# Performance work log

Measured on AMD Instinct MI355X. Metric: run time of the kernel, lower is better.

## Reference

```python
import jax, jax.numpy as jnp
import numpy as np

# physics constants (match init_kwargs)
DT = 1.0 / 60.0
G_ACC = 9.81
RHO = 1.225
CD = 0.47
NU = 0.001
B, N, GRID = 512, 64, 16


def _norm(x):
    return jnp.linalg.norm(x, axis=-1, keepdims=True)


def _deriv(pos, vel, rot, omega, mass, inertia, contacts, fluid_v,
           Fext, tau, log_A, log_k, log_b, conv_w):
    g_vec = jnp.array([0.0, 0.0, -G_ACC], dtype=pos.dtype)
    Fg = mass[..., None] * g_vec                                  # [B,N,3]
    A = jax.nn.softplus(log_A).reshape(1, -1, 1)
    vm = jnp.maximum(_norm(vel), 1e-6)
    Fd = -0.5 * RHO * CD * A * vm * vel                           # drag
    k = jax.nn.softplus(log_k)
    b = jax.nn.softplus(log_b)
    d_ij = pos[:, None, :, :] - pos[:, :, None, :]                # [B,N,N,3] = p_j - p_i
    dist = jnp.maximum(_norm(d_ij), 1e-6)
    n_hat = d_ij / dist
    pen = jax.nn.relu(1.0 - dist[..., 0])                         # penetration depth
    dvel = vel[:, None, :, :] - vel[:, :, None, :]                # v_j - v_i
    Fc = (k * pen[..., None] * n_hat + b * dvel * contacts[..., None]).sum(axis=2)
    dv = (Fext + Fg + Fd + Fc) / mass[..., None]
    Io = inertia * omega
    domega = (tau - jnp.cross(omega, Io)) / jnp.maximum(inertia, 1e-6)
    w, x, y, z = rot[..., 0], rot[..., 1], rot[..., 2], rot[..., 3]
    ox, oy, oz = omega[..., 0], omega[..., 1], omega[..., 2]
    drot = 0.5 * jnp.stack([
        -x * ox - y * oy - z * oz,
        w * ox + y * oz - z * oy,
        w * oy - x * oz + z * ox,
        w * oz + x * oy - y * ox], axis=-1)
    P_in = (Fext * vel).sum((-1, -2))
    P_dis = -(Fd * vel).sum((-1, -2))
    dE = P_in - P_dis
    Bsz = fluid_v.shape[0]
    u = fluid_v.reshape(Bsz, GRID, GRID, GRID, 3).transpose(0, 4, 1, 2, 3)  # NCDHW
    dfluid = NU * jax.lax.conv_general_dilated(
        u, conv_w, window_strides=(1, 1, 1), padding=[(1, 1)] * 3,
        feature_group_count=3,
        dimension_numbers=('NCDHW', 'OIDHW', 'NCDHW'))
    dfluid = dfluid.transpose(0, 2, 3, 4, 1).reshape(Bsz, GRID ** 3, 3)
    return vel, dv, drot, domega, dE, dfluid


def _quat_normalize(q):
    return q / jnp.maximum(_norm(q), 1e-12)


def _apply(pos, vel, rot, omega, fluid_v, dt, dp, dv, dr, dw, dfluid):
    npos = pos + dt * dp
    nvel = vel + dt * dv
    nrot = _quat_normalize(rot + dt * dr)
    nomega = omega + dt * dw
    new_u = fluid_v + dt * dfluid
    nfluid = new_u - new_u.mean(axis=1, keepdims=True)
    return npos, nvel, nrot, nomega, nfluid


def _forward(pos, vel, rot, omega, mass, inertia, contacts, energy, fluid_v,
             Fext, tau, log_A, log_k, log_b, conv_w):
    dt = DT
    params = (mass, inertia, contacts)

    def deriv(p, v, r, o, fv):
        return _deriv(p, v, r, o, mass, inertia, contacts, fv,
                      Fext, tau, log_A, log_k, log_b, conv_w)

    k1 = deriv(pos, vel, rot, omega, fluid_v)
    s2 = _apply(pos, vel, rot, omega, fluid_v, dt / 2, k1[0], k1[1], k1[2], k1[3], k1[5])
    k2 = deriv(*s2)
    s3 = _apply(pos, vel, rot, omega, fluid_v, dt / 2, k2[0], k2[1], k2[2], k2[3], k2[5])
    k3 = deriv(*s3)
    s4 = _apply(pos, vel, rot, omega, fluid_v, dt, k3[0], k3[1], k3[2], k3[3], k3[5])
    k4 = deriv(*s4)

    def rk4c(y, a, b_, c, d):
        return y + dt / 6 * (a + 2 * b_ + 2 * c + d)

    npos = rk4c(pos, k1[0], k2[0], k3[0], k4[0])
    nvel = rk4c(vel, k1[1], k2[1], k3[1], k4[1])
    nrot = _quat_normalize(rk4c(rot, k1[2], k2[2], k3[2], k4[2]))
    nomega = rk4c(omega, k1[3], k2[3], k3[3], k4[3])
    nenergy = rk4c(energy, k1[4], k2[4], k3[4], k4[4])
    nforces = Fext + mass[..., None] * k1[1]
    raw_fluid = rk4c(fluid_v, k1[5], k2[5], k3[5], k4[5])
    nfluid = raw_fluid - raw_fluid.mean(axis=1, keepdims=True)
    Bsz = pos.shape[0]
    # flatten new state: [pos, vel, rot, omega, forces, energy, fluid_v]
    return jnp.concatenate([
        npos.reshape(Bsz, -1), nvel.reshape(Bsz, -1), nrot.reshape(Bsz, -1),
        nomega.reshape(Bsz, -1), nforces.reshape(Bsz, -1),
        nenergy[:, None], nfluid.reshape(Bsz, -1)], axis=-1)


def setup_inputs() -> dict:
    key = jax.random.key(0)
    ks = jax.random.split(key, 12)
    rot = jax.random.normal(ks[2], (B, N, 4), dtype=jnp.float32)
    rot = rot / jnp.maximum(jnp.linalg.norm(rot, axis=-1, keepdims=True), 1e-12)
    return {
        'pos': 2.0 * jax.random.normal(ks[0], (B, N, 3), dtype=jnp.float32),
        'vel': jax.random.normal(ks[1], (B, N, 3), dtype=jnp.float32),
        'rot': rot,
        'omega': jax.random.normal(ks[3], (B, N, 3), dtype=jnp.float32),
        'mass': 0.5 + jax.random.uniform(ks[4], (B, N), dtype=jnp.float32),
        'inertia': 0.05 + 0.1 * jax.random.uniform(ks[5], (B, N, 3), dtype=jnp.float32),
        'contacts': jax.random.uniform(ks[6], (B, N, N), dtype=jnp.float32),
        'energy': jnp.zeros((B,), dtype=jnp.float32),
        'fluid_v': jax.random.normal(ks[7], (B, GRID ** 3, 3), dtype=jnp.float32),
        'Fext': jax.random.normal(ks[8], (B, N, 3), dtype=jnp.float32),
        'tau': jax.random.normal(ks[9], (B, N, 3), dtype=jnp.float32),
        'log_A': jnp.zeros((N,), dtype=jnp.float32),
        'log_k': jnp.full((1,), np.log(1000.0), dtype=jnp.float32),
        'log_b': jnp.full((1,), np.log(10.0), dtype=jnp.float32),
        'conv_w': 0.1 * jax.random.normal(ks[10], (3, 1, 3, 3, 3), dtype=jnp.float32),
    }


def reference(pos, vel, rot, omega, mass, inertia, contacts, energy, fluid_v,
              Fext, tau, log_A, log_k, log_b, conv_w):
    return _forward(pos, vel, rot, omega, mass, inertia, contacts, energy,
                    fluid_v, Fext, tau, log_A, log_k, log_b, conv_w)
```

## Files before the change

kernel.cpp:

```cpp
#include <hip/hip_runtime.h>

#define DT (1.0f/60.0f)
#define G_ACC 9.81f
#define RHO 1.225f
#define CD_ 0.47f
#define NU 0.001f

__device__ __forceinline__ float softplus_f(float x) {
    return log1pf(expf(-fabsf(x))) + fmaxf(x, 0.0f);
}

#define RL(v, l) __int_as_float(__builtin_amdgcn_readlane(__float_as_int(v), (l)))
#define SLANE(x) __int_as_float(__builtin_amdgcn_readfirstlane(__float_as_int(x)))

__device__ __forceinline__ float dpp_xm(float v) {
    return __int_as_float(__builtin_amdgcn_update_dpp(0, __float_as_int(v), 0x111, 0xf, 0xf, true));
}
__device__ __forceinline__ float dpp_xp(float v) {
    return __int_as_float(__builtin_amdgcn_update_dpp(0, __float_as_int(v), 0x101, 0xf, 0xf, true));
}

__global__ __launch_bounds__(512) void fused_kernel(
    const float* __restrict__ pos, const float* __restrict__ vel,
    const float* __restrict__ rot, const float* __restrict__ omega,
    const float* __restrict__ mass, const float* __restrict__ inertia,
    const float* __restrict__ contacts, const float* __restrict__ energy,
    const float* __restrict__ fluid, const float* __restrict__ Fext,
    const float* __restrict__ tau, const float* __restrict__ log_A,
    const float* __restrict__ log_k, const float* __restrict__ log_b,
    const float* __restrict__ conv_w, float* __restrict__ out)
{
    __shared__ float smem[8772];
    const int t = threadIdx.x;

    if (blockIdx.x < 1536) {
        const int b   = blockIdx.x & 511;
        const int ch  = blockIdx.x >> 9;
        const int col = t & 255;
        const int h   = t >> 8;
        const int x   = col & 15, y = col >> 4, wv = t >> 6;
        const int h8  = h << 3;
        float* red = smem + 8740;

        float W[27];
        #pragma unroll
        for (int k = 0; k < 27; ++k) W[k] = NU * SLANE(conv_w[ch*27 + k]);

        const int lb = col*17;
        if (t < 18) { smem[4352 + t] = 0.f; smem[4370 + 4352 + t] = 0.f; }

        const float* fb = fluid + (size_t)b*12288 + 3*col + ch;
        float base[8], acc[8];
        #pragma unroll
        for (int zz = 0; zz < 8; ++zz) {
            float v = fb[(h8 + zz)*768];
            base[zz] = v; acc[zz] = 0.f;
            smem[lb + h8 + zz] = v;
        }

        const float xm = (x > 0) ? 1.f : 0.f, xp = (x < 15) ? 1.f : 0.f;
        const float mm = (y > 0) ? 1.f : 0.f, pm = (y < 15) ? 1.f : 0.f;
        float Sdz0, Sdz1, Sdz2;
        {
            float a0 = W[0]*xm + W[1] + W[2]*xp;
            float a1 = W[3]*xm + W[4] + W[5]*xp;
            float a2 = W[6]*xm + W[7] + W[8]*xp;
            Sdz0 = mm*a0 + a1 + pm*a2;
            a0 = W[ 9]*xm + W[10] + W[11]*xp;
            a1 = W[12]*xm + W[13] + W[14]*xp;
            a2 = W[15]*xm + W[16] + W[17]*xp;
            Sdz1 = mm*a0 + a1 + pm*a2;
            a0 = W[18]*xm + W[19] + W[20]*xp;
            a1 = W[21]*xm + W[22] + W[23]*xp;
            a2 = W[24]*xm + W[25] + W[26]*xp;
            Sdz2 = mm*a0 + a1 + pm*a2;
        }
        const float SzLo = Sdz1 + Sdz2;
        const float SzHi = Sdz0 + Sdz1;
        const float SzMid = Sdz0 + Sdz1 + Sdz2;

        const int ownR = lb + h8 - 1;
        const int cmR  = (y > 0)  ? (lb - 272 + h8 - 1) : 4353;
        const int cpR  = (y < 15) ? (lb + 272 + h8 - 1) : 4353;

        __syncthreads();
        float mean = 0.f;

        #define LOADC(cidx) { \
            const float* Up = smem + rb + (cidx); \
            if (h == 0) { c[0] = 0.f; \
                _Pragma("unroll") for (int k = 1; k < 10; ++k) c[k] = Up[k]; } \
            else { \
                _Pragma("unroll") for (int k = 0; k < 9; ++k) c[k] = Up[k]; \
                c[9] = 0.f; } }

        #define SCAT(wy) { \
            _Pragma("unroll") for (int k = 0; k < 10; ++k) { \
                float cc = c[k], cl = dpp_xm(cc), cr = dpp_xp(cc); \
                if (k < 8) \
                    o[k]   += W[(wy)*3+0]*cl + W[(wy)*3+1]*cc + W[(wy)*3+2]*cr; \
                if (k >= 1 && k <= 8) \
                    o[k-1] += W[9+(wy)*3+0]*cl + W[9+(wy)*3+1]*cc + W[9+(wy)*3+2]*cr; \
                if (k >= 2) \
                    o[k-2] += W[18+(wy)*3+0]*cl + W[18+(wy)*3+1]*cc + W[18+(wy)*3+2]*cr; \
            } }

        #pragma unroll
        for (int s = 0; s < 4; ++s) {
            const int rb = (s & 1) * 4370;
            const int wb = 4370 - rb;
            float o[8];
            #pragma unroll
            for (int zz = 0; zz < 8; ++zz) o[zz] = 0.f;
            {
                float c[10];
                LOADC(ownR); SCAT(1);
                LOADC(cmR);  SCAT(0);
                LOADC(cpR);  SCAT(2);
            }

            if (s < 3) {
                const float hstep = (s == 2) ? DT : DT*0.5f;
                const float w = (s == 0) ? 1.f : 2.f;
                float ps = 0.f;
                #pragma unroll
                for (int zz = 0; zz < 8; ++zz) {
                    float Sz = (h == 0 && zz == 0) ? SzLo
                             : ((h == 1 && zz == 7) ? SzHi : SzMid);
                    float k = o[zz] - mean * Sz;
                    acc[zz] += w * k;
                    float v = base[zz] + hstep * k;
                    smem[wb + lb + h8 + zz] = v;
                    ps += v;
                }
                #pragma unroll
                for (int off = 32; off > 0; off >>= 1) ps += __shfl_xor(ps, off, 64);
                if ((t & 63) == 0) red[s*8 + wv] = ps;
                __syncthreads();
                mean = (red[s*8+0]+red[s*8+1]+red[s*8+2]+red[s*8+3]
                       +red[s*8+4]+red[s*8+5]+red[s*8+6]+red[s*8+7]) * (1.0f/4096.0f);
            } else {
                #pragma unroll
                for (int zz = 0; zz < 8; ++zz) {
                    float Sz = (h == 0 && zz == 0) ? SzLo
                             : ((h == 1 && zz == 7) ? SzHi : SzMid);
                    acc[zz] += o[zz] - mean * Sz;
                }
            }
        }
        #undef LOADC
        #undef SCAT

        float raw[8], ps = 0.f;
        #pragma unroll
        for (int zz = 0; zz < 8; ++zz) { raw[zz] = base[zz] + (DT/6.0f)*acc[zz]; ps += raw[zz]; }
        #pragma unroll
        for (int off = 32; off > 0; off >>= 1) ps += __shfl_xor(ps, off, 64);
        if ((t & 63) == 0) red[24 + wv] = ps;
        __syncthreads();
        const float mn = (red[24]+red[25]+red[26]+red[27]
                         +red[28]+red[29]+red[30]+red[31]) * (1.0f/4096.0f);

        float* ob = out + (size_t)b*13313 + 1025 + 3*col + ch;
        #pragma unroll
        for (int zz = 0; zz < 8; ++zz) ob[(h8 + zz)*768] = raw[zz] - mn;
        return;
    }

    const int b = blockIdx.x - 1536;
    const int q = t >> 6;
    const int i = t & 63;
    float* cont = smem;
    float* sF   = smem + 4160;

    {
        const float4* cg = (const float4*)(contacts + (size_t)b*4096);
        #pragma unroll
        for (int v = 0; v < 2; ++v) {
            float4 c4 = cg[v*512 + t];
            int fi = (v*512 + t) * 4;
            int r = fi >> 6, cc = fi & 63;
            float* p = cont + r*65 + cc;
            p[0] = c4.x; p[1] = c4.y; p[2] = c4.z; p[3] = c4.w;
        }
    }

    const size_t p3 = ((size_t)b*64 + i)*3;
    const size_t p4 = ((size_t)b*64 + i)*4;
    float bpx=pos[p3],   bpy=pos[p3+1],   bpz=pos[p3+2];
    float bvx=vel[p3],   bvy=vel[p3+1],   bvz=vel[p3+2];
    float brw=rot[p4],   brx=rot[p4+1],   bry=rot[p4+2],  brz=rot[p4+3];
    float box=omega[p3], boy=omega[p3+1], boz=omega[p3+2];
    float m  = mass[(size_t)b*64+i];
    float Ix=inertia[p3], Iy=inertia[p3+1], Iz=inertia[p3+2];
    float Fex=Fext[p3],   Fey=Fext[p3+1],   Fez=Fext[p3+2];
    float tx=tau[p3],     ty=tau[p3+1],     tz=tau[p3+2];
    float dragc = -0.5f * RHO * CD_ * softplus_f(log_A[i]);
    float kc = softplus_f(SLANE(log_k[0]));
    float bc = softplus_f(SLANE(log_b[0]));
    float invm = 1.0f / m;
    float iIx = 1.0f/fmaxf(Ix,1e-6f), iIy = 1.0f/fmaxf(Iy,1e-6f), iIz = 1.0f/fmaxf(Iz,1e-6f);

    float cpx=bpx, cpy=bpy, cpz=bpz;
    float cvx=bvx, cvy=bvy, cvz=bvz;
    float crw=brw, crx=brx, cry=bry, crz=brz;
    float cox=box, coy=boy, coz=boz;

    float apx=0,apy=0,apz=0, avx=0,avy=0,avz=0;
    float arw=0,arx=0,ary=0,arz=0, awx=0,awy=0,awz=0;
    float eacc=0.f;

    const int j0 = q << 3;
    float* ob = out + (size_t)b * 13313;
    __syncthreads();

    #pragma unroll
    for (int s = 0; s < 4; ++s) {
        float Fcx=0.f, Fcy=0.f, Fcz=0.f;
        #pragma unroll
        for (int jj = 0; jj < 8; ++jj) {
            const int j = j0 + jj;
            float pjx = RL(cpx, j), pjy = RL(cpy, j), pjz = RL(cpz, j);
            float vjx = RL(cvx, j), vjy = RL(cvy, j), vjz = RL(cvz, j);
            float dx = pjx - cpx, dy = pjy - cpy, dz = pjz - cpz;
            float dist = fmaxf(sqrtf(dx*dx + dy*dy + dz*dz), 1e-6f);
            float pen  = fmaxf(1.0f - dist, 0.0f);
            float coef = kc * pen * __builtin_amdgcn_rcpf(dist);
            float cbj  = bc * cont[i*65 + j];
            Fcx += coef*dx + cbj*(vjx - cvx);
            Fcy += coef*dy + cbj*(vjy - cvy);
            Fcz += coef*dz + cbj*(vjz - cvz);
        }
        sF[q*192 + i*3+0] = Fcx;
        sF[q*192 + i*3+1] = Fcy;
        sF[q*192 + i*3+2] = Fcz;
        __syncthreads();
        Fcx = 0.f; Fcy = 0.f; Fcz = 0.f;
        #pragma unroll
        for (int qq = 0; qq < 8; ++qq) {
            Fcx += sF[qq*192 + i*3+0];
            Fcy += sF[qq*192 + i*3+1];
            Fcz += sF[qq*192 + i*3+2];
        }

        float vm = fmaxf(sqrtf(cvx*cvx+cvy*cvy+cvz*cvz), 1e-6f);
        float dc = dragc * vm;
        float Fdx = dc*cvx, Fdy = dc*cvy, Fdz = dc*cvz;

        float dvx = (Fex + Fdx + Fcx) * invm;
        float dvy = (Fey + Fdy + Fcy) * invm;
        float dvz = (Fez - m*G_ACC + Fdz + Fcz) * invm;

        if (s == 0 && q == 0) {
            ob[832 + i*3+0] = Fex + m*dvx;
            ob[832 + i*3+1] = Fey + m*dvy;
            ob[832 + i*3+2] = Fez + m*dvz;
        }

        float dqw = 0.5f*(-crx*cox - cry*coy - crz*coz);
        float dqx = 0.5f*( crw*cox + cry*coz - crz*coy);
        float dqy = 0.5f*( crw*coy - crx*coz + crz*cox);
        float dqz = 0.5f*( crw*coz + crx*coy - cry*cox);

        float Iox = Ix*cox, Ioy = Iy*coy, Ioz = Iz*coz;
        float dwx = (tx - (coy*Ioz - coz*Ioy)) * iIx;
        float dwy = (ty - (coz*Iox - cox*Ioz)) * iIy;
        float dwz = (tz - (cox*Ioy - coy*Iox)) * iIz;

        float ei = (Fex+Fdx)*cvx + (Fey+Fdy)*cvy + (Fez+Fdz)*cvz;
        #pragma unroll
        for (int off = 32; off > 0; off >>= 1) ei += __shfl_xor(ei, off, 64);

        const float w = (s == 0 || s == 3) ? 1.f : 2.f;
        eacc += w * ei;
        apx += w*cvx; apy += w*cvy; apz += w*cvz;
        avx += w*dvx; avy += w*dvy; avz += w*dvz;
        arw += w*dqw; arx += w*dqx; ary += w*dqy; arz += w*dqz;
        awx += w*dwx; awy += w*dwy; awz += w*dwz;

        if (s < 3) {
            const float h = (s == 2) ? DT : DT*0.5f;
            float npx = bpx + h*cvx, npy = bpy + h*cvy, npz = bpz + h*cvz;
            cvx = bvx + h*dvx; cvy = bvy + h*dvy; cvz = bvz + h*dvz;
            cpx = npx; cpy = npy; cpz = npz;
            float qw = brw + h*dqw, qx = brx + h*dqx, qy = bry + h*dqy, qz = brz + h*dqz;
            float iqn = 1.0f / fmaxf(sqrtf(qw*qw+qx*qx+qy*qy+qz*qz), 1e-12f);
            crw = qw*iqn; crx = qx*iqn; cry = qy*iqn; crz = qz*iqn;
            cox = box + h*dwx; coy = boy + h*dwy; coz = boz + h*dwz;
            __syncthreads();
        }
    }

    if (q == 0) {
        const float s6 = DT / 6.0f;
        ob[      i*3+0] = bpx + s6*apx;  ob[      i*3+1] = bpy + s6*apy;  ob[      i*3+2] = bpz + s6*apz;
        ob[192 + i*3+0] = bvx + s6*avx;  ob[192 + i*3+1] = bvy + s6*avy;  ob[192 + i*3+2] = bvz + s6*avz;
        {
            float qw=brw+s6*arw, qx=brx+s6*arx, qy=bry+s6*ary, qz=brz+s6*arz;
            float iq = 1.0f / fmaxf(sqrtf(qw*qw+qx*qx+qy*qy+qz*qz), 1e-12f);
            ob[384 + i*4+0]=qw*iq; ob[384 + i*4+1]=qx*iq; ob[384 + i*4+2]=qy*iq; ob[384 + i*4+3]=qz*iq;
        }
        ob[640 + i*3+0] = box + s6*awx;  ob[640 + i*3+1] = boy + s6*awy;  ob[640 + i*3+2] = boz + s6*awz;
        if (i == 0) ob[1024] = energy[b] + s6*eacc;
    }
}

extern "C" void kernel_launch(void* const* d_in, const int* in_sizes, int n_in,
                              void* d_out, int out_size, void* d_ws, size_t ws_size,
                              hipStream_t stream) {
    const float* pos      = (const float*)d_in[0];
    const float* vel      = (const float*)d_in[1];
    const float* rot      = (const float*)d_in[2];
    const float* omega    = (const float*)d_in[3];
    const float* mass     = (const float*)d_in[4];
    const float* inertia  = (const float*)d_in[5];
    const float* contacts = (const float*)d_in[6];
    const float* energy   = (const float*)d_in[7];
    const float* fluid_v  = (const float*)d_in[8];
    const float* Fext     = (const float*)d_in[9];
    const float* tau      = (const float*)d_in[10];
    const float* log_A    = (const float*)d_in[11];
    const float* log_k    = (const float*)d_in[12];
    const float* log_b    = (const float*)d_in[13];
    const float* conv_w   = (const float*)d_in[14];
    float* out = (float*)d_out;

    fused_kernel<<<dim3(2048), dim3(512), 0, stream>>>(
        pos, vel, rot, omega, mass, inertia, contacts, energy, fluid_v,
        Fext, tau, log_A, log_k, log_b, conv_w, out);
}
```

Measured before the change: 182.3 us.

## Single-buffer fluid stencil LDS and keep own column in registers

```diff
diff --git a/kernel.cpp b/kernel.cpp
--- a/kernel.cpp
+++ b/kernel.cpp
@@ -30,7 +30,7 @@
     const float* __restrict__ log_k, const float* __restrict__ log_b,
     const float* __restrict__ conv_w, float* __restrict__ out)
 {
-    __shared__ float smem[8772];
+    __shared__ float smem[5696];
     const int t = threadIdx.x;
 
     if (blockIdx.x < 1536) {
@@ -40,22 +40,23 @@
         const int h   = t >> 8;
         const int x   = col & 15, y = col >> 4, wv = t >> 6;
         const int h8  = h << 3;
-        float* red = smem + 8740;
+        float* u   = smem;
+        float* red = smem + 4370;
+
+        if (t < 18) u[4352 + t] = 0.f;
 
         float W[27];
         #pragma unroll
         for (int k = 0; k < 27; ++k) W[k] = NU * SLANE(conv_w[ch*27 + k]);
 
         const int lb = col*17;
-        if (t < 18) { smem[4352 + t] = 0.f; smem[4370 + 4352 + t] = 0.f; }
-
         const float* fb = fluid + (size_t)b*12288 + 3*col + ch;
-        float base[8], acc[8];
+        float base[8], acc[8], f[8];
         #pragma unroll
         for (int zz = 0; zz < 8; ++zz) {
             float v = fb[(h8 + zz)*768];
-            base[zz] = v; acc[zz] = 0.f;
-            smem[lb + h8 + zz] = v;
+            base[zz] = v; acc[zz] = 0.f; f[zz] = v;
+            u[lb + h8 + zz] = v;
         }
 
         const float xm = (x > 0) ? 1.f : 0.f, xp = (x < 15) ? 1.f : 0.f;
@@ -79,44 +80,39 @@
         const float SzHi = Sdz0 + Sdz1;
         const float SzMid = Sdz0 + Sdz1 + Sdz2;
 
-        const int ownR = lb + h8 - 1;
-        const int cmR  = (y > 0)  ? (lb - 272 + h8 - 1) : 4353;
-        const int cpR  = (y < 15) ? (lb + 272 + h8 - 1) : 4353;
+        const int cmO = ((y > 0)  ? lb - 272 : 4353) + h8 - 1;
+        const int cpO = ((y < 15) ? lb + 272 : 4353) + h8 - 1;
 
         __syncthreads();
         float mean = 0.f;
 
-        #define LOADC(cidx) { \
-            const float* Up = smem + rb + (cidx); \
-            if (h == 0) { c[0] = 0.f; \
-                _Pragma("unroll") for (int k = 1; k < 10; ++k) c[k] = Up[k]; } \
-            else { \
-                _Pragma("unroll") for (int k = 0; k < 9; ++k) c[k] = Up[k]; \
-                c[9] = 0.f; } }
-
-        #define SCAT(wy) { \
-            _Pragma("unroll") for (int k = 0; k < 10; ++k) { \
-                float cc = c[k], cl = dpp_xm(cc), cr = dpp_xp(cc); \
-                if (k < 8) \
-                    o[k]   += W[(wy)*3+0]*cl + W[(wy)*3+1]*cc + W[(wy)*3+2]*cr; \
-                if (k >= 1 && k <= 8) \
-                    o[k-1] += W[9+(wy)*3+0]*cl + W[9+(wy)*3+1]*cc + W[9+(wy)*3+2]*cr; \
-                if (k >= 2) \
-                    o[k-2] += W[18+(wy)*3+0]*cl + W[18+(wy)*3+1]*cc + W[18+(wy)*3+2]*cr; \
-            } }
+        #define ACCK(c, wy) { \
+            float cl_ = dpp_xm(c), cr_ = dpp_xp(c); \
+            if (k < 8) \
+                o[k]   += W[(wy)*3]*cl_ + W[(wy)*3+1]*(c) + W[(wy)*3+2]*cr_; \
+            if (k >= 1 && k <= 8) \
+                o[k-1] += W[9+(wy)*3]*cl_ + W[9+(wy)*3+1]*(c) + W[9+(wy)*3+2]*cr_; \
+            if (k >= 2) \
+                o[k-2] += W[18+(wy)*3]*cl_ + W[18+(wy)*3+1]*(c) + W[18+(wy)*3+2]*cr_; \
+        }
 
         #pragma unroll
         for (int s = 0; s < 4; ++s) {
-            const int rb = (s & 1) * 4370;
-            const int wb = 4370 - rb;
+            float hal = u[lb + (h ? 7 : 8)];
             float o[8];
             #pragma unroll
             for (int zz = 0; zz < 8; ++zz) o[zz] = 0.f;
-            {
-                float c[10];
-                LOADC(ownR); SCAT(1);
-                LOADC(cmR);  SCAT(0);
-                LOADC(cpR);  SCAT(2);
+
+            #pragma unroll
+            for (int k = 0; k < 10; ++k) {
+                if (!((h == 0 && k == 0) || (h == 1 && k == 9))) {
+                    float ov = (k == 0 || k == 9) ? hal : f[k-1];
+                    float cv = u[cmO + k];
+                    float pv = u[cpO + k];
+                    ACCK(ov, 1);
+                    ACCK(cv, 0);
+                    ACCK(pv, 2);
+                }
             }
 
             if (s < 3) {
@@ -127,18 +123,20 @@
                 for (int zz = 0; zz < 8; ++zz) {
                     float Sz = (h == 0 && zz == 0) ? SzLo
                              : ((h == 1 && zz == 7) ? SzHi : SzMid);
-                    float k = o[zz] - mean * Sz;
-                    acc[zz] += w * k;
-                    float v = base[zz] + hstep * k;
-                    smem[wb + lb + h8 + zz] = v;
-                    ps += v;
+                    float kk = o[zz] - mean * Sz;
+                    acc[zz] += w * kk;
+                    f[zz] = base[zz] + hstep * kk;
+                    ps += f[zz];
                 }
                 #pragma unroll
                 for (int off = 32; off > 0; off >>= 1) ps += __shfl_xor(ps, off, 64);
-                if ((t & 63) == 0) red[s*8 + wv] = ps;
                 __syncthreads();
-                mean = (red[s*8+0]+red[s*8+1]+red[s*8+2]+red[s*8+3]
-                       +red[s*8+4]+red[s*8+5]+red[s*8+6]+red[s*8+7]) * (1.0f/4096.0f);
+                #pragma unroll
+                for (int zz = 0; zz < 8; ++zz) u[lb + h8 + zz] = f[zz];
+                if ((t & 63) == 0) red[wv] = ps;
+                __syncthreads();
+                mean = (red[0]+red[1]+red[2]+red[3]
+                       +red[4]+red[5]+red[6]+red[7]) * (1.0f/4096.0f);
             } else {
                 #pragma unroll
                 for (int zz = 0; zz < 8; ++zz) {
@@ -148,18 +146,18 @@
                 }
             }
         }
-        #undef LOADC
-        #undef SCAT
+        #undef ACCK
 
         float raw[8], ps = 0.f;
         #pragma unroll
         for (int zz = 0; zz < 8; ++zz) { raw[zz] = base[zz] + (DT/6.0f)*acc[zz]; ps += raw[zz]; }
         #pragma unroll
         for (int off = 32; off > 0; off >>= 1) ps += __shfl_xor(ps, off, 64);
-        if ((t & 63) == 0) red[24 + wv] = ps;
         __syncthreads();
-        const float mn = (red[24]+red[25]+red[26]+red[27]
-                         +red[28]+red[29]+red[30]+red[31]) * (1.0f/4096.0f);
+        if ((t & 63) == 0) red[wv] = ps;
+        __syncthreads();
+        const float mn = (red[0]+red[1]+red[2]+red[3]
+                         +red[4]+red[5]+red[6]+red[7]) * (1.0f/4096.0f);
 
         float* ob = out + (size_t)b*13313 + 1025 + 3*col + ch;
         #pragma unroll
```

Result: no change. 184.8 us (+1.4%).
